# Performance work log

Measured on AMD Instinct MI355X. Metric: run time of the kernel, lower is better.

## Reference

```python
import jax, jax.numpy as jnp
import numpy as np

KERN = 2  # matches init kwarg


def _avgpool(x):
    # non-overlapping avg pool kernel=stride=KERN on (N,C,H,W)
    N, C, H, W = x.shape
    return x.reshape(N, C, H // KERN, KERN, W // KERN, KERN).mean(axis=(3, 5))


def _pair_sum(mu1, var1, mu2, var2):
    # mu*, var*: (N, D). Broadcast to (N, N, D) and reduce to scalar.
    d = mu1[:, None, :] - mu2[None, :, :]
    s = var1[:, None, :] + var2[None, :, :]
    return jnp.sum(jnp.exp(-0.5 * (d * d / s + jnp.log(s))))


def setup_inputs() -> dict:
    key = jax.random.key(0)
    k1, k2, k3, k4 = jax.random.split(key, 4)
    shp = (128, 16, 32, 32)
    return {
        "mu_a": jax.random.normal(k1, shp, dtype=jnp.float32),
        "logvar_a": jax.random.normal(k2, shp, dtype=jnp.float32),
        "mu_b": jax.random.normal(k3, shp, dtype=jnp.float32),
        "logvar_b": jax.random.normal(k4, shp, dtype=jnp.float32),
    }


def reference(mu_a, logvar_a, mu_b, logvar_b):
    inv_k2 = 1.0 / (KERN * KERN)
    ma = _avgpool(mu_a)
    mb = _avgpool(mu_b)
    va = _avgpool(jnp.exp(logvar_a)) * inv_k2
    vb = _avgpool(jnp.exp(logvar_b)) * inv_k2
    N = ma.shape[0]
    ma, mb = ma.reshape(N, -1), mb.reshape(N, -1)
    va, vb = va.reshape(N, -1), vb.reshape(N, -1)
    vaa = _pair_sum(ma, va, ma, va)
    vab = _pair_sum(ma, va, mb, vb)
    vbb = _pair_sum(mb, vb, mb, vb)
    return vaa + vbb - 2.0 * vab
```

## Files before the change

kernel.cpp:

```cpp
#include <hip/hip_runtime.h>

#define NN 128
#define CC_ 16
#define HH 32
#define WW 32
#define DD 4096
#define ND (NN*DD)

typedef float v2f __attribute__((ext_vector_type(2)));

#define MU_SCALE 0.8493218002880191f

__global__ __launch_bounds__(256) void pool_kernel(
    const float* __restrict__ mu_a, const float* __restrict__ lv_a,
    const float* __restrict__ mu_b, const float* __restrict__ lv_b,
    float2* __restrict__ wm, float2* __restrict__ wv, float* __restrict__ out)
{
    int t = blockIdx.x * 256 + threadIdx.x;
    if (t == 0) out[0] = 0.0f;

    int wo = t & 15;
    int ho = (t >> 4) & 15;
    int c  = (t >> 8) & 15;
    int n  = t >> 12;

    int base = ((n * CC_ + c) * HH + 2 * ho) * WW + 2 * wo;

    float2 a0 = *(const float2*)(mu_a + base);
    float2 a1 = *(const float2*)(mu_a + base + WW);
    float2 la0 = *(const float2*)(lv_a + base);
    float2 la1 = *(const float2*)(lv_a + base + WW);
    float2 b0 = *(const float2*)(mu_b + base);
    float2 b1 = *(const float2*)(mu_b + base + WW);
    float2 lb0 = *(const float2*)(lv_b + base);
    float2 lb1 = *(const float2*)(lv_b + base + WW);

    const float ms = 0.25f * MU_SCALE;
    float ma_v = ms * (a0.x + a0.y + a1.x + a1.y);
    float mb_v = ms * (b0.x + b0.y + b1.x + b1.y);
    float va_v = 0.0625f * (__expf(la0.x) + __expf(la0.y) + __expf(la1.x) + __expf(la1.y));
    float vb_v = 0.0625f * (__expf(lb0.x) + __expf(lb0.y) + __expf(lb1.x) + __expf(lb1.y));

    wm[t] = make_float2(ma_v, mb_v);
    wv[t] = make_float2(va_v, vb_v);
}

#define JCHUNK 32

__device__ __forceinline__ void pair_group(
    v2f& acc, v2f mi, v2f mj, v2f vi, v2f vj)
{
    v2f dd = mi - mj;
    v2f s  = vi + vj;
    v2f r;
    r.x = __builtin_amdgcn_rsqf(s.x);
    r.y = __builtin_amdgcn_rsqf(s.y);
    v2f q  = dd * r;
    v2f qq = q * q;
    v2f e;
    e.x = __builtin_amdgcn_exp2f(-qq.x);
    e.y = __builtin_amdgcn_exp2f(-qq.y);
    acc += e * r;
}

__global__ __launch_bounds__(256) void pair_kernel(
    const float2* __restrict__ wm, const float2* __restrict__ wv,
    float* __restrict__ out)
{
    const int d  = blockIdx.x * 256 + threadIdx.x;
    const int i0 = (blockIdx.y >> 2) * 4;
    const int j0 = (blockIdx.y & 3) * JCHUNK;

    v2f pma[2], pmb[2], pva[2], pvb[2];
#pragma unroll
    for (int p = 0; p < 2; ++p) {
        float2 m0 = wm[(i0 + 2 * p) * DD + d];
        float2 m1 = wm[(i0 + 2 * p + 1) * DD + d];
        float2 v0 = wv[(i0 + 2 * p) * DD + d];
        float2 v1 = wv[(i0 + 2 * p + 1) * DD + d];
        pma[p] = (v2f){m0.x, m1.x};
        pmb[p] = (v2f){m0.y, m1.y};
        pva[p] = (v2f){v0.x, v1.x};
        pvb[p] = (v2f){v0.y, v1.y};
    }

    v2f acc_aa = (v2f){0.0f, 0.0f};
    v2f acc_bb = (v2f){0.0f, 0.0f};
    v2f acc_ab = (v2f){0.0f, 0.0f};

#pragma unroll 2
    for (int j = j0; j < j0 + JCHUNK; ++j) {
        float2 jm = wm[j * DD + d];
        float2 jv = wv[j * DD + d];
        v2f jma2 = (v2f){jm.x, jm.x};
        v2f jmb2 = (v2f){jm.y, jm.y};
        v2f jva2 = (v2f){jv.x, jv.x};
        v2f jvb2 = (v2f){jv.y, jv.y};
#pragma unroll
        for (int p = 0; p < 2; ++p) {
            pair_group(acc_aa, pma[p], jma2, pva[p], jva2);
            pair_group(acc_bb, pmb[p], jmb2, pvb[p], jvb2);
            pair_group(acc_ab, pma[p], jmb2, pva[p], jvb2);
        }
    }

    float part = (acc_aa.x + acc_aa.y) + (acc_bb.x + acc_bb.y)
               - 2.0f * (acc_ab.x + acc_ab.y);

#pragma unroll
    for (int off = 32; off > 0; off >>= 1)
        part += __shfl_down(part, off, 64);

    __shared__ float wsum[4];
    int lane = threadIdx.x & 63;
    int wv_  = threadIdx.x >> 6;
    if (lane == 0) wsum[wv_] = part;
    __syncthreads();
    if (threadIdx.x == 0) {
        float s = wsum[0] + wsum[1] + wsum[2] + wsum[3];
        atomicAdd(out, s);
    }
}

extern "C" void kernel_launch(void* const* d_in, const int* in_sizes, int n_in,
                              void* d_out, int out_size, void* d_ws, size_t ws_size,
                              hipStream_t stream) {
    const float* mu_a = (const float*)d_in[0];
    const float* lv_a = (const float*)d_in[1];
    const float* mu_b = (const float*)d_in[2];
    const float* lv_b = (const float*)d_in[3];
    float* out = (float*)d_out;
    float2* wm = (float2*)d_ws;
    float2* wv = ((float2*)d_ws) + ND;

    pool_kernel<<<dim3(ND / 256), 256, 0, stream>>>(mu_a, lv_a, mu_b, lv_b, wm, wv, out);
    pair_kernel<<<dim3(DD / 256, (NN / 4) * (NN / JCHUNK)), 256, 0, stream>>>(wm, wv, out);
}
```

Measured before the change: 123.8 us.

## Exploit symmetry of aa/bb pair sums to skip half the pair evaluations

Uses the symmetry of the aa and bb pair sums to compute only the lower triangle, with the diagonal weighted by one half, then doubles the result. The j loop is split into three ranges: fully below the i block (all three terms), a diagonal band with per-pair weights, and above the block (cross term only). This targets roughly a third of the exp/rsq work. In exchange, work becomes uneven across blocks, since some blocks do much less than others.

```diff
diff --git a/kernel.cpp b/kernel.cpp
--- a/kernel.cpp
+++ b/kernel.cpp
@@ -63,6 +63,23 @@
     acc += e * r;
 }
 
+__device__ __forceinline__ void pair_group_w(
+    v2f& acc, v2f w, v2f mi, v2f mj, v2f vi, v2f vj)
+{
+    v2f dd = mi - mj;
+    v2f s  = vi + vj;
+    v2f r;
+    r.x = __builtin_amdgcn_rsqf(s.x);
+    r.y = __builtin_amdgcn_rsqf(s.y);
+    v2f q  = dd * r;
+    v2f qq = q * q;
+    v2f e;
+    e.x = __builtin_amdgcn_exp2f(-qq.x);
+    e.y = __builtin_amdgcn_exp2f(-qq.y);
+    v2f er = e * r;
+    acc += w * er;
+}
+
 __global__ __launch_bounds__(256) void pair_kernel(
     const float2* __restrict__ wm, const float2* __restrict__ wv,
     float* __restrict__ out)
@@ -70,6 +87,7 @@
     const int d  = blockIdx.x * 256 + threadIdx.x;
     const int i0 = (blockIdx.y >> 2) * 4;
     const int j0 = (blockIdx.y & 3) * JCHUNK;
+    const int hi = j0 + JCHUNK;
 
     v2f pma[2], pmb[2], pva[2], pvb[2];
 #pragma unroll
@@ -88,8 +106,13 @@
     v2f acc_bb = (v2f){0.0f, 0.0f};
     v2f acc_ab = (v2f){0.0f, 0.0f};
 
+    const int below_end = min(hi, i0);
+    const int band_lo   = max(j0, i0);
+    const int band_hi   = min(hi, i0 + 4);
+    const int above_lo  = max(j0, i0 + 4);
+
 #pragma unroll 2
-    for (int j = j0; j < j0 + JCHUNK; ++j) {
+    for (int j = j0; j < below_end; ++j) {
         float2 jm = wm[j * DD + d];
         float2 jv = wv[j * DD + d];
         v2f jma2 = (v2f){jm.x, jm.x};
@@ -104,8 +127,42 @@
         }
     }
 
-    float part = (acc_aa.x + acc_aa.y) + (acc_bb.x + acc_bb.y)
-               - 2.0f * (acc_ab.x + acc_ab.y);
+    for (int j = band_lo; j < band_hi; ++j) {
+        float2 jm = wm[j * DD + d];
+        float2 jv = wv[j * DD + d];
+        v2f jma2 = (v2f){jm.x, jm.x};
+        v2f jmb2 = (v2f){jm.y, jm.y};
+        v2f jva2 = (v2f){jv.x, jv.x};
+        v2f jvb2 = (v2f){jv.y, jv.y};
+        v2f w[2];
+#pragma unroll
+        for (int p = 0; p < 2; ++p) {
+            int r0 = i0 + 2 * p, r1 = r0 + 1;
+            w[p].x = (j < r0) ? 1.0f : (j == r0 ? 0.5f : 0.0f);
+            w[p].y = (j < r1) ? 1.0f : (j == r1 ? 0.5f : 0.0f);
+        }
+#pragma unroll
+        for (int p = 0; p < 2; ++p) {
+            pair_group_w(acc_aa, w[p], pma[p], jma2, pva[p], jva2);
+            pair_group_w(acc_bb, w[p], pmb[p], jmb2, pvb[p], jvb2);
+            pair_group(acc_ab, pma[p], jmb2, pva[p], jvb2);
+        }
+    }
+
+#pragma unroll 2
+    for (int j = above_lo; j < hi; ++j) {
+        float2 jm = wm[j * DD + d];
+        float2 jv = wv[j * DD + d];
+        v2f jmb2 = (v2f){jm.y, jm.y};
+        v2f jvb2 = (v2f){jv.y, jv.y};
+#pragma unroll
+        for (int p = 0; p < 2; ++p) {
+            pair_group(acc_ab, pma[p], jmb2, pva[p], jvb2);
+        }
+    }
+
+    float part = 2.0f * ((acc_aa.x + acc_aa.y) + (acc_bb.x + acc_bb.y)
+                       - (acc_ab.x + acc_ab.y));
 
 #pragma unroll
     for (int off = 32; off > 0; off >>= 1)
```

Measured after the change: 123.8 us. About the same (+0.1%).

## Exploit symmetry of self-pair sums via triangular tiling of i,j blocks

Applied to the files above, without the earlier changes.

The aa and bb pair sums are symmetric in i and j, so the kernel now computes only the upper triangle of 8x8 tiles (136 tile pairs), doubling off-diagonal contributions and weighting the diagonal tiles. The ab cross term keeps its own rectangular blocks. This removes nearly half of the exp/rsq work for the self terms, at the cost of wasted lanes on the masked diagonal tiles, divergent block types and a sqrt-based triangular index decode.

```diff
diff --git a/kernel.cpp b/kernel.cpp
--- a/kernel.cpp
+++ b/kernel.cpp
@@ -45,8 +45,6 @@
     wv[t] = make_float2(va_v, vb_v);
 }
 
-#define JCHUNK 32
-
 __device__ __forceinline__ void pair_group(
     v2f& acc, v2f mi, v2f mj, v2f vi, v2f vj)
 {
@@ -63,49 +61,104 @@
     acc += e * r;
 }
 
+__device__ __forceinline__ void pair_group_w(
+    v2f& acc, float w, v2f mi, v2f mj, v2f vi, v2f vj)
+{
+    v2f dd = mi - mj;
+    v2f s  = vi + vj;
+    v2f r;
+    r.x = __builtin_amdgcn_rsqf(s.x);
+    r.y = __builtin_amdgcn_rsqf(s.y);
+    v2f q  = dd * r;
+    v2f qq = q * q;
+    v2f e;
+    e.x = __builtin_amdgcn_exp2f(-qq.x);
+    e.y = __builtin_amdgcn_exp2f(-qq.y);
+    v2f er = e * r;
+    acc += (v2f){w, w} * er;
+}
+
 __global__ __launch_bounds__(256) void pair_kernel(
     const float2* __restrict__ wm, const float2* __restrict__ wv,
     float* __restrict__ out)
 {
-    const int d  = blockIdx.x * 256 + threadIdx.x;
-    const int i0 = (blockIdx.y >> 2) * 4;
-    const int j0 = (blockIdx.y & 3) * JCHUNK;
+    const int d = blockIdx.x * 256 + threadIdx.x;
+    const int y = blockIdx.y;
 
-    v2f pma[2], pmb[2], pva[2], pvb[2];
+    float part;
+
+    if (y < 136) {
+        int ti = (int)((sqrtf(8.0f * (float)y + 1.0f) - 1.0f) * 0.5f + 1e-4f);
+        int tj = y - ti * (ti + 1) / 2;
+        const int i0 = ti * 8, j0 = tj * 8;
+
+        v2f pm[8], pv[8];
 #pragma unroll
-    for (int p = 0; p < 2; ++p) {
-        float2 m0 = wm[(i0 + 2 * p) * DD + d];
-        float2 m1 = wm[(i0 + 2 * p + 1) * DD + d];
-        float2 v0 = wv[(i0 + 2 * p) * DD + d];
-        float2 v1 = wv[(i0 + 2 * p + 1) * DD + d];
-        pma[p] = (v2f){m0.x, m1.x};
-        pmb[p] = (v2f){m0.y, m1.y};
-        pva[p] = (v2f){v0.x, v1.x};
-        pvb[p] = (v2f){v0.y, v1.y};
-    }
+        for (int p = 0; p < 8; ++p) {
+            float2 m = wm[(i0 + p) * DD + d];
+            float2 v = wv[(i0 + p) * DD + d];
+            pm[p] = (v2f){m.x, m.y};
+            pv[p] = (v2f){v.x, v.y};
+        }
 
-    v2f acc_aa = (v2f){0.0f, 0.0f};
-    v2f acc_bb = (v2f){0.0f, 0.0f};
-    v2f acc_ab = (v2f){0.0f, 0.0f};
+        v2f acc = (v2f){0.0f, 0.0f};
+        if (ti != tj) {
+#pragma unroll 2
+            for (int jj = 0; jj < 8; ++jj) {
+                float2 mjf = wm[(j0 + jj) * DD + d];
+                float2 vjf = wv[(j0 + jj) * DD + d];
+                v2f mj = (v2f){mjf.x, mjf.y};
+                v2f vj = (v2f){vjf.x, vjf.y};
+#pragma unroll
+                for (int p = 0; p < 8; ++p)
+                    pair_group(acc, pm[p], mj, pv[p], vj);
+            }
+        } else {
+#pragma unroll 2
+            for (int jj = 0; jj < 8; ++jj) {
+                float2 mjf = wm[(j0 + jj) * DD + d];
+                float2 vjf = wv[(j0 + jj) * DD + d];
+                v2f mj = (v2f){mjf.x, mjf.y};
+                v2f vj = (v2f){vjf.x, vjf.y};
+                int j = j0 + jj;
+#pragma unroll
+                for (int p = 0; p < 8; ++p) {
+                    int i = i0 + p;
+                    float w = (j < i) ? 1.0f : ((j == i) ? 0.5f : 0.0f);
+                    pair_group_w(acc, w, pm[p], mj, pv[p], vj);
+                }
+            }
+        }
+        part = 2.0f * (acc.x + acc.y);
+    } else {
+        const int y2 = y - 136;
+        const int i0 = (y2 >> 2) * 4;
+        const int j0 = (y2 & 3) * 32;
 
-#pragma unroll 2
-    for (int j = j0; j < j0 + JCHUNK; ++j) {
-        float2 jm = wm[j * DD + d];
-        float2 jv = wv[j * DD + d];
-        v2f jma2 = (v2f){jm.x, jm.x};
-        v2f jmb2 = (v2f){jm.y, jm.y};
-        v2f jva2 = (v2f){jv.x, jv.x};
-        v2f jvb2 = (v2f){jv.y, jv.y};
+        v2f pma[2], pva[2];
 #pragma unroll
         for (int p = 0; p < 2; ++p) {
-            pair_group(acc_aa, pma[p], jma2, pva[p], jva2);
-            pair_group(acc_bb, pmb[p], jmb2, pvb[p], jvb2);
-            pair_group(acc_ab, pma[p], jmb2, pva[p], jvb2);
+            float2 m0 = wm[(i0 + 2 * p) * DD + d];
+            float2 m1 = wm[(i0 + 2 * p + 1) * DD + d];
+            float2 v0 = wv[(i0 + 2 * p) * DD + d];
+            float2 v1 = wv[(i0 + 2 * p + 1) * DD + d];
+            pma[p] = (v2f){m0.x, m1.x};
+            pva[p] = (v2f){v0.x, v1.x};
         }
+
+        v2f acc = (v2f){0.0f, 0.0f};
+#pragma unroll 2
+        for (int j = j0; j < j0 + 32; ++j) {
+            float2 jm = wm[j * DD + d];
+            float2 jv = wv[j * DD + d];
+            v2f jmb2 = (v2f){jm.y, jm.y};
+            v2f jvb2 = (v2f){jv.y, jv.y};
+#pragma unroll
+            for (int p = 0; p < 2; ++p)
+                pair_group(acc, pma[p], jmb2, pva[p], jvb2);
+        }
+        part = -2.0f * (acc.x + acc.y);
     }
-
-    float part = (acc_aa.x + acc_aa.y) + (acc_bb.x + acc_bb.y)
-               - 2.0f * (acc_ab.x + acc_ab.y);
 
 #pragma unroll
     for (int off = 32; off > 0; off >>= 1)
@@ -134,5 +187,5 @@
     float2* wv = ((float2*)d_ws) + ND;
 
     pool_kernel<<<dim3(ND / 256), 256, 0, stream>>>(mu_a, lv_a, mu_b, lv_b, wm, wv, out);
-    pair_kernel<<<dim3(DD / 256, (NN / 4) * (NN / JCHUNK)), 256, 0, stream>>>(wm, wv, out);
+    pair_kernel<<<dim3(DD / 256, 136 + 128), 256, 0, stream>>>(wm, wv, out);
 }
```

New measurement: 139.2 us. 1.12x slower.
